# Performance work log

Hardware: AMD Instinct MI355X
Metric: run time of the kernel (lower is better)

## Reference

```python
import jax, jax.numpy as jnp
import numpy as np

DIM = 4096
CAP = 8192
EPS = 1e-8  # torch F.cosine_similarity denominator clamp


def setup_inputs() -> dict:
    key = jax.random.key(0)
    k1, k2, k3, k4, k5, k6 = jax.random.split(key, 6)
    return {
        "query": jax.random.normal(k1, (DIM,), dtype=jnp.float32),
        "memory_bank": jax.random.normal(k2, (CAP, DIM), dtype=jnp.float32),
        "importance": jax.random.uniform(k3, (CAP,), dtype=jnp.float32),
        "age": jax.random.uniform(k4, (CAP,), dtype=jnp.float32) * 1000.0,
        "W_dec": jax.random.normal(k5, (DIM, DIM), dtype=jnp.float32) * (1.0 / np.sqrt(DIM)),
        "b_dec": jax.random.normal(k6, (DIM,), dtype=jnp.float32) * 0.01,
        "top_k": 8,
    }


def reference(query, memory_bank, importance, age, W_dec, b_dec, top_k):
    # Cosine similarity of query against every memory row (torch semantics:
    # dot / max(||q||*||m||, eps)).
    dots = memory_bank @ query                       # [CAP]
    qn = jnp.sqrt(jnp.sum(query * query))
    mn = jnp.sqrt(jnp.sum(memory_bank * memory_bank, axis=1))
    sim = dots / jnp.maximum(qn * mn, EPS)
    # Time-decayed importance weighting.
    weighted = sim * importance * jnp.exp(-0.001 * age)
    # Top-k retrieval, mean-pool retrieved rows, decode.
    _, idx = jax.lax.top_k(weighted, top_k)          # [k]
    retrieved = jnp.mean(memory_bank[idx], axis=0)   # [DIM]
    return retrieved @ W_dec.T + b_dec
```

## Files before the change

### kernel.cpp

```cpp
#include <hip/hip_runtime.h>
#include <math.h>

#define DIM 4096
#define CAP 8192
#define EPS 1e-8f

__global__ __launch_bounds__(256) void score_kernel(
    const float* __restrict__ q,
    const float* __restrict__ mb,
    const float* __restrict__ imp,
    const float* __restrict__ age,
    float* __restrict__ weighted)
{
    const int wave = threadIdx.x >> 6;
    const int lane = threadIdx.x & 63;
    const int row  = (blockIdx.x << 2) + wave;

    const float4* __restrict__ mrow = (const float4*)(mb + (size_t)row * DIM);
    const float4* __restrict__ q4   = (const float4*)q;

    float dot = 0.f, msq = 0.f, qsq = 0.f;
    #pragma unroll 4
    for (int i = lane; i < DIM / 4; i += 64) {
        float4 m  = mrow[i];
        float4 qq = q4[i];
        dot = fmaf(m.w, qq.w, fmaf(m.z, qq.z, fmaf(m.y, qq.y, fmaf(m.x, qq.x, dot))));
        msq = fmaf(m.w, m.w,  fmaf(m.z, m.z,  fmaf(m.y, m.y,  fmaf(m.x, m.x,  msq))));
        qsq = fmaf(qq.w, qq.w, fmaf(qq.z, qq.z, fmaf(qq.y, qq.y, fmaf(qq.x, qq.x, qsq))));
    }
    #pragma unroll
    for (int off = 32; off > 0; off >>= 1) {
        dot += __shfl_down(dot, off, 64);
        msq += __shfl_down(msq, off, 64);
        qsq += __shfl_down(qsq, off, 64);
    }
    if (lane == 0) {
        float denom = fmaxf(sqrtf(qsq) * sqrtf(msq), EPS);
        weighted[row] = (dot / denom) * imp[row] * expf(-0.001f * age[row]);
    }
}

__global__ __launch_bounds__(512) void topk_gather_kernel(
    const float* __restrict__ weighted,
    const float* __restrict__ mb,
    const int* __restrict__ topk_ptr,
    float* __restrict__ retrieved)
{
    __shared__ float wv[CAP];
    __shared__ float rv[8];
    __shared__ int   ri[8];
    __shared__ int   sidx[64];

    const int tid  = threadIdx.x;
    const int wave = tid >> 6;
    const int lane = tid & 63;

    {
        const float4* __restrict__ w4  = (const float4*)weighted;
        float4* __restrict__       wv4 = (float4*)wv;
        #pragma unroll
        for (int i = tid; i < CAP / 4; i += 512) wv4[i] = w4[i];
    }
    __syncthreads();

    int k = *topk_ptr;
    if (k < 1) k = 1;
    if (k > 64) k = 64;

    float bv = -INFINITY; int bi = tid;
    #pragma unroll
    for (int j = 0; j < CAP / 512; ++j) {
        const int idx = tid + (j << 9);
        const float v = wv[idx];
        if (v > bv) { bv = v; bi = idx; }
    }

    for (int it = 0; it < k; ++it) {
        float cv = bv; int ci = bi;
        #pragma unroll
        for (int off = 32; off > 0; off >>= 1) {
            float ov = __shfl_down(cv, off, 64);
            int   oi = __shfl_down(ci, off, 64);
            if (ov > cv || (ov == cv && oi < ci)) { cv = ov; ci = oi; }
        }
        if (lane == 0) { rv[wave] = cv; ri[wave] = ci; }
        __syncthreads();
        if (tid == 0) {
            float best = rv[0]; int besti = ri[0];
            #pragma unroll
            for (int w = 1; w < 8; ++w) {
                if (rv[w] > best || (rv[w] == best && ri[w] < besti)) {
                    best = rv[w]; besti = ri[w];
                }
            }
            sidx[it] = besti;
            wv[besti] = -INFINITY;
        }
        __syncthreads();
        const int gbi = sidx[it];
        if ((gbi & 511) == tid) {
            bv = -INFINITY; bi = tid;
            #pragma unroll
            for (int j = 0; j < CAP / 512; ++j) {
                const int idx = tid + (j << 9);
                const float v = wv[idx];
                if (v > bv) { bv = v; bi = idx; }
            }
        }
    }
    __syncthreads();

    const float inv_k = 1.0f / (float)k;
    for (int i = tid; i < DIM / 4; i += 512) {
        float4 acc = make_float4(0.f, 0.f, 0.f, 0.f);
        for (int r = 0; r < k; ++r) {
            const float4 v = ((const float4*)(mb + (size_t)sidx[r] * DIM))[i];
            acc.x += v.x; acc.y += v.y; acc.z += v.z; acc.w += v.w;
        }
        acc.x *= inv_k; acc.y *= inv_k; acc.z *= inv_k; acc.w *= inv_k;
        ((float4*)retrieved)[i] = acc;
    }
}

__global__ __launch_bounds__(256) void decode_kernel(
    const float* __restrict__ W,
    const float* __restrict__ b,
    const float* __restrict__ r,
    float* __restrict__ out)
{
    const int wave = threadIdx.x >> 6;
    const int lane = threadIdx.x & 63;
    const int j    = (blockIdx.x << 2) + wave;

    const float4* __restrict__ wrow = (const float4*)(W + (size_t)j * DIM);
    const float4* __restrict__ r4   = (const float4*)r;

    float acc = 0.f;
    #pragma unroll 4
    for (int i = lane; i < DIM / 4; i += 64) {
        float4 w = wrow[i];
        float4 v = r4[i];
        acc = fmaf(w.w, v.w, fmaf(w.z, v.z, fmaf(w.y, v.y, fmaf(w.x, v.x, acc))));
    }
    #pragma unroll
    for (int off = 32; off > 0; off >>= 1) acc += __shfl_down(acc, off, 64);
    if (lane == 0) out[j] = acc + b[j];
}

extern "C" void kernel_launch(void* const* d_in, const int* in_sizes, int n_in,
                              void* d_out, int out_size, void* d_ws, size_t ws_size,
                              hipStream_t stream) {
    const float* query      = (const float*)d_in[0];
    const float* memory     = (const float*)d_in[1];
    const float* importance = (const float*)d_in[2];
    const float* age        = (const float*)d_in[3];
    const float* W_dec      = (const float*)d_in[4];
    const float* b_dec      = (const float*)d_in[5];
    const int*   top_k      = (const int*)d_in[6];

    float* weighted  = (float*)d_ws;
    float* retrieved = (float*)d_ws + CAP;
    float* out       = (float*)d_out;

    score_kernel<<<CAP / 4, 256, 0, stream>>>(query, memory, importance, age, weighted);
    topk_gather_kernel<<<1, 512, 0, stream>>>(weighted, memory, top_k, retrieved);
    decode_kernel<<<DIM / 4, 256, 0, stream>>>(W_dec, b_dec, retrieved, out);
}
```

Baseline: 260.2 us.

## Fuse top-k and gather into decode, recomputing selection redundantly per block

Merges the single-block top-k/gather kernel and the decode kernel into one kernel launched across all decode blocks. Each block redundantly reads the weighted scores into registers, runs the iterative top-k, and mean-pools the selected memory rows into shared memory before computing its four output rows. This removes the serial single-block stage, one launch, and the global round trip of the retrieved vector. In exchange, every one of the 1024 blocks repeats the top-k and the k-row gather (mostly served from cache), which adds redundant work and latency to each block.

```diff
diff --git a/kernel.cpp b/kernel.cpp
--- a/kernel.cpp
+++ b/kernel.cpp
@@ -40,39 +40,40 @@
     }
 }
 
-__global__ __launch_bounds__(512) void topk_gather_kernel(
+__global__ __launch_bounds__(256) void topk_decode_kernel(
     const float* __restrict__ weighted,
     const float* __restrict__ mb,
     const int* __restrict__ topk_ptr,
-    float* __restrict__ retrieved)
+    const float* __restrict__ W,
+    const float* __restrict__ b,
+    float* __restrict__ out)
 {
-    __shared__ float wv[CAP];
-    __shared__ float rv[8];
-    __shared__ int   ri[8];
+    __shared__ float rbar[DIM];
+    __shared__ float rv[4];
+    __shared__ int   ri[4];
     __shared__ int   sidx[64];
 
     const int tid  = threadIdx.x;
     const int wave = tid >> 6;
     const int lane = tid & 63;
 
-    {
-        const float4* __restrict__ w4  = (const float4*)weighted;
-        float4* __restrict__       wv4 = (float4*)wv;
-        #pragma unroll
-        for (int i = tid; i < CAP / 4; i += 512) wv4[i] = w4[i];
-    }
-    __syncthreads();
-
     int k = *topk_ptr;
     if (k < 1) k = 1;
     if (k > 64) k = 64;
 
-    float bv = -INFINITY; int bi = tid;
+    const float4* __restrict__ w4 = (const float4*)weighted;
+    float4 val[8];
     #pragma unroll
-    for (int j = 0; j < CAP / 512; ++j) {
-        const int idx = tid + (j << 9);
-        const float v = wv[idx];
-        if (v > bv) { bv = v; bi = idx; }
+    for (int j = 0; j < 8; ++j) val[j] = w4[(j << 8) + tid];
+
+    float bv = -INFINITY; int bi = 0x7fffffff;
+    #pragma unroll
+    for (int j = 0; j < 8; ++j) {
+        const int base = (j << 10) + (tid << 2);
+        if (val[j].x > bv) { bv = val[j].x; bi = base + 0; }
+        if (val[j].y > bv) { bv = val[j].y; bi = base + 1; }
+        if (val[j].z > bv) { bv = val[j].z; bi = base + 2; }
+        if (val[j].w > bv) { bv = val[j].w; bi = base + 3; }
     }
 
     for (int it = 0; it < k; ++it) {
@@ -88,58 +89,61 @@
         if (tid == 0) {
             float best = rv[0]; int besti = ri[0];
             #pragma unroll
-            for (int w = 1; w < 8; ++w) {
+            for (int w = 1; w < 4; ++w) {
                 if (rv[w] > best || (rv[w] == best && ri[w] < besti)) {
                     best = rv[w]; besti = ri[w];
                 }
             }
             sidx[it] = besti;
-            wv[besti] = -INFINITY;
         }
         __syncthreads();
         const int gbi = sidx[it];
-        if ((gbi & 511) == tid) {
-            bv = -INFINITY; bi = tid;
+        if (((gbi >> 2) & 255) == tid) {
+            const int jr = gbi >> 10;
+            const int cr = gbi & 3;
             #pragma unroll
-            for (int j = 0; j < CAP / 512; ++j) {
-                const int idx = tid + (j << 9);
-                const float v = wv[idx];
-                if (v > bv) { bv = v; bi = idx; }
+            for (int j = 0; j < 8; ++j) {
+                if (j == jr) {
+                    if (cr == 0) val[j].x = -INFINITY;
+                    if (cr == 1) val[j].y = -INFINITY;
+                    if (cr == 2) val[j].z = -INFINITY;
+                    if (cr == 3) val[j].w = -INFINITY;
+                }
+            }
+            bv = -INFINITY; bi = 0x7fffffff;
+            #pragma unroll
+            for (int j = 0; j < 8; ++j) {
+                const int base = (j << 10) + (tid << 2);
+                if (val[j].x > bv) { bv = val[j].x; bi = base + 0; }
+                if (val[j].y > bv) { bv = val[j].y; bi = base + 1; }
+                if (val[j].z > bv) { bv = val[j].z; bi = base + 2; }
+                if (val[j].w > bv) { bv = val[j].w; bi = base + 3; }
             }
         }
     }
     __syncthreads();
 
     const float inv_k = 1.0f / (float)k;
-    for (int i = tid; i < DIM / 4; i += 512) {
+    float4* __restrict__ rbar4 = (float4*)rbar;
+    for (int i = tid; i < DIM / 4; i += 256) {
         float4 acc = make_float4(0.f, 0.f, 0.f, 0.f);
         for (int r = 0; r < k; ++r) {
             const float4 v = ((const float4*)(mb + (size_t)sidx[r] * DIM))[i];
             acc.x += v.x; acc.y += v.y; acc.z += v.z; acc.w += v.w;
         }
         acc.x *= inv_k; acc.y *= inv_k; acc.z *= inv_k; acc.w *= inv_k;
-        ((float4*)retrieved)[i] = acc;
+        rbar4[i] = acc;
     }
-}
+    __syncthreads();
 
-__global__ __launch_bounds__(256) void decode_kernel(
-    const float* __restrict__ W,
-    const float* __restrict__ b,
-    const float* __restrict__ r,
-    float* __restrict__ out)
-{
-    const int wave = threadIdx.x >> 6;
-    const int lane = threadIdx.x & 63;
-    const int j    = (blockIdx.x << 2) + wave;
-
+    const int j = (blockIdx.x << 2) + wave;
     const float4* __restrict__ wrow = (const float4*)(W + (size_t)j * DIM);
-    const float4* __restrict__ r4   = (const float4*)r;
 
     float acc = 0.f;
     #pragma unroll 4
     for (int i = lane; i < DIM / 4; i += 64) {
         float4 w = wrow[i];
-        float4 v = r4[i];
+        float4 v = rbar4[i];
         acc = fmaf(w.w, v.w, fmaf(w.z, v.z, fmaf(w.y, v.y, fmaf(w.x, v.x, acc))));
     }
     #pragma unroll
@@ -158,11 +162,10 @@
     const float* b_dec      = (const float*)d_in[5];
     const int*   top_k      = (const int*)d_in[6];
 
-    float* weighted  = (float*)d_ws;
-    float* retrieved = (float*)d_ws + CAP;
-    float* out       = (float*)d_out;
+    float* weighted = (float*)d_ws;
+    float* out      = (float*)d_out;
 
     score_kernel<<<CAP / 4, 256, 0, stream>>>(query, memory, importance, age, weighted);
-    topk_gather_kernel<<<1, 512, 0, stream>>>(weighted, memory, top_k, retrieved);
-    decode_kernel<<<DIM / 4, 256, 0, stream>>>(W_dec, b_dec, retrieved, out);
+    topk_decode_kernel<<<DIM / 4, 256, 0, stream>>>(weighted, memory, top_k,
+                                                    W_dec, b_dec, out);
 }
```

New measurement: 254.7 us. 1.02x faster.
